# Kernel tuning notes

Hardware: AMD Instinct MI355X
Metric: run time of the kernel (lower is better)

## Reference

```python
import jax, jax.numpy as jnp
import numpy as np

CUTOFF = 5.0
ENV_EXP = 5          # envelope_exponent
NUM_RADIAL = 6
EMB = 128
NUM_ATOM_TYPES = 95
N_NODES = 50000
N_EDGES = 800000


def envelope(x):
    # p = exponent + 1
    p = ENV_EXP + 1
    a = -(p + 1) * (p + 2) / 2.0
    b = p * (p + 2) * 1.0
    c = -p * (p + 1) / 2.0
    x_p_0 = x ** (p - 1)
    x_p_1 = x_p_0 * x
    x_p_2 = x_p_1 * x
    return 1.0 / x + a * x_p_0 + b * x_p_1 + c * x_p_2


def setup_inputs() -> dict:
    key = jax.random.key(0)
    ks = jax.random.split(key, 10)
    Z = jax.random.randint(ks[0], (N_NODES,), 0, NUM_ATOM_TYPES)
    src = jax.random.randint(ks[1], (N_EDGES,), 0, N_NODES)
    dst = jax.random.randint(ks[2], (N_EDGES,), 0, N_NODES)
    rbf = jax.random.normal(ks[3], (N_EDGES, NUM_RADIAL), dtype=jnp.float32)
    # distances in (0, cutoff]; keep away from 0 to avoid 1/x blowup
    d = jax.random.uniform(ks[4], (N_EDGES,), dtype=jnp.float32,
                           minval=0.05, maxval=1.0) * CUTOFF
    sqrt3 = float(np.sqrt(3.0))
    emb_table = jax.random.uniform(ks[5], (NUM_ATOM_TYPES, EMB),
                                   dtype=jnp.float32, minval=-sqrt3, maxval=sqrt3)
    W_rbf = jax.random.normal(ks[6], (EMB, NUM_RADIAL), dtype=jnp.float32) * (1.0 / np.sqrt(NUM_RADIAL))
    b_rbf = jnp.zeros((EMB,), dtype=jnp.float32)
    W_dense = jax.random.normal(ks[7], (EMB, 3 * EMB), dtype=jnp.float32) * (1.0 / np.sqrt(3 * EMB))
    b_dense = jnp.zeros((EMB,), dtype=jnp.float32)
    return {"Z": Z, "src": src, "dst": dst, "rbf": rbf, "d": d,
            "emb_table": emb_table, "W_rbf": W_rbf, "b_rbf": b_rbf,
            "W_dense": W_dense, "b_dense": b_dense}


def reference(Z, src, dst, rbf, d, emb_table, W_rbf, b_rbf, W_dense, b_dense):
    act = jax.nn.silu
    # node embeddings: g.ndata['h'] = embedding(Z)
    h = emb_table[Z]                                   # [N, EMB]
    # edge_init
    rbf_proj = act(rbf @ W_rbf.T + b_rbf)              # [E, EMB]
    m = jnp.concatenate([h[src], h[dst], rbf_proj], axis=-1)  # [E, 3*EMB]
    m = act(m @ W_dense.T + b_dense)                   # [E, EMB]
    d_scaled = d / CUTOFF                              # [E]
    # bessel funcs: sin(n*pi*x)/x, n = 1..NUM_RADIAL (stacked along dim=1)
    freqs = jnp.pi * jnp.arange(1, NUM_RADIAL + 1, dtype=d.dtype)  # [R]
    rbf_env = jnp.sin(d_scaled[:, None] * freqs) / d_scaled[:, None]  # [E, R]
    d_cutoff = envelope(d_scaled)                      # [E]
    rbf_env = d_cutoff[:, None] * rbf_env              # [E, R]
    return h, m, rbf_env
```

## Files before the change

kernel.cpp:

```cpp
#include <hip/hip_runtime.h>
#include <hip/hip_bf16.h>
#include <math.h>

#define CUTOFFV 5.0f
#define NRAD 6
#define EMB 128
#define NTYPES 95
#define PI_F 3.14159265358979323846f

typedef short short8 __attribute__((ext_vector_type(8)));
typedef float f32x4 __attribute__((ext_vector_type(4)));
typedef float f32x2 __attribute__((ext_vector_type(2)));

__device__ __forceinline__ unsigned short f2bf(float f) {
    union { float f; unsigned int u; } v; v.f = f;
    unsigned int u = v.u;
    unsigned int r = (u + 0x7FFFu + ((u >> 16) & 1u)) >> 16;
    return (unsigned short)r;
}

__device__ __forceinline__ short bf16s(float f) {
    union { __hip_bfloat16 h; short s; } u;
    u.h = __float2bfloat16(f);
    return u.s;
}

__device__ __forceinline__ float fast_rcp(float x) {
    float y;
    asm("v_rcp_f32 %0, %1" : "=v"(y) : "v"(x));
    return y;
}

__device__ __forceinline__ float silu_f(float x) {
    return x * fast_rcp(1.0f + __expf(-x));
}

__device__ __forceinline__ void lds_barrier() {
    __builtin_amdgcn_sched_barrier(0);
    asm volatile("s_waitcnt lgkmcnt(0)\n\ts_barrier" ::: "memory");
    __builtin_amdgcn_sched_barrier(0);
}

__global__ void prep_kernel(const float* __restrict__ emb,
                            const float* __restrict__ Wd,
                            const float* __restrict__ bd,
                            const float* __restrict__ Wr,
                            const float* __restrict__ brbf,
                            float* __restrict__ P1, float* __restrict__ P2,
                            unsigned short* __restrict__ W3b,
                            float* __restrict__ Wrp) {
    int b = blockIdx.x, tid = threadIdx.x;
    if (b < 2 * NTYPES) {
        int t = b / NTYPES, z = b % NTYPES;
        __shared__ float emb_s[EMB];
        emb_s[tid] = emb[z * EMB + tid];
        __syncthreads();
        float acc = (t == 0) ? bd[tid] : 0.0f;
        const float* wrow = Wd + (size_t)tid * 384 + t * EMB;
        #pragma unroll 8
        for (int j = 0; j < EMB; ++j) acc += emb_s[j] * wrow[j];
        (t == 0 ? P1 : P2)[z * EMB + tid] = acc;
    } else if (b < 2 * NTYPES + 8) {
        int g = (b - 2 * NTYPES) * 128 + tid;
        for (int i = g; i < EMB * EMB; i += 8 * 128) {
            int n = i >> 7, k = i & 127;
            W3b[i] = f2bf(Wd[(size_t)n * 384 + 256 + k]);
        }
    } else {
        if (tid < EMB) {
            int k = tid;
            #pragma unroll
            for (int j = 0; j < 6; ++j) Wrp[k * 8 + j] = Wr[k * 6 + j];
            Wrp[k * 8 + 6] = brbf[k];
            Wrp[k * 8 + 7] = 0.0f;
        }
    }
}

__global__ void __launch_bounds__(256, 4)
edge_kernel(const int* __restrict__ Z, const int* __restrict__ src,
            const int* __restrict__ dst, const float* __restrict__ rbf,
            const float* __restrict__ dvec, const float* __restrict__ emb,
            const float* __restrict__ P1, const float* __restrict__ P2,
            const unsigned short* __restrict__ W3b,
            const float* __restrict__ Wrp,
            float* __restrict__ out_h, float* __restrict__ out_m,
            float* __restrict__ out_env,
            int N, int E, int ntiles) {
    __shared__ unsigned char A_lds[2][64 * 256];
    __shared__ int zs_s[2][64], zd_s[2][64];

    const int tid = threadIdx.x;
    const int lane = tid & 63;
    const int w = tid >> 6;
    const int lr = lane & 15;
    const int lg = lane >> 4;
    const int wu = __builtin_amdgcn_readfirstlane(w);

    {
        const int total_h = N * (EMB / 4);
        const f32x4* e4 = (const f32x4*)emb;
        for (int idx = blockIdx.x * 256 + tid; idx < total_h;
             idx += gridDim.x * 256) {
            int v = idx >> 5, c = idx & 31;
            __builtin_nontemporal_store(e4[Z[v] * 32 + c], (f32x4*)out_h + idx);
        }
    }
    for (int e = blockIdx.x * 256 + tid; e < E; e += gridDim.x * 256) {
        float x = dvec[e] * (1.0f / CUTOFFV);
        float inv = fast_rcp(x);
        float x2 = x * x;
        float x5 = x2 * x2 * x;
        float env = inv + x5 * (-28.0f + x * (48.0f - 21.0f * x));
        float s1, c1;
        __sincosf(PI_F * x, &s1, &c1);
        float twoc = 2.0f * c1;
        float f = env * inv;
        float s2 = twoc * s1;
        float s3 = twoc * s2 - s1;
        float s4 = twoc * s3 - s2;
        float s5 = twoc * s4 - s3;
        float s6 = twoc * s5 - s4;
        float* o = out_env + (size_t)e * 6;
        __builtin_nontemporal_store((f32x2){f * s1, f * s2}, (f32x2*)o);
        __builtin_nontemporal_store((f32x2){f * s3, f * s4}, (f32x2*)(o + 2));
        __builtin_nontemporal_store((f32x2){f * s5, f * s6}, (f32x2*)(o + 4));
    }

    short8 wfrag[2][4];
    #pragma unroll
    for (int nt = 0; nt < 2; ++nt) {
        int n = w * 32 + nt * 16 + lr;
        #pragma unroll
        for (int ks = 0; ks < 4; ++ks)
            wfrag[nt][ks] = *(const short8*)(W3b + n * EMB + ks * 32 + lg * 8);
    }

    for (int i = 0; ; ++i) {
        const int tp = blockIdx.x + i * gridDim.x;
        const int tc = tp - gridDim.x;
        const bool do_p = (tp < ntiles);
        const bool do_c = (i > 0) && (tc < ntiles);
        if (!do_p && !do_c) break;
        const int pi = i & 1, ci = pi ^ 1;

        f32x2 ra = {0.f, 0.f}, rb = {0.f, 0.f}, rc = {0.f, 0.f};
        int iv = 0;
        if (do_p) {
            const int e0p = tp * 64;
            int ecl = e0p + lane; if (ecl >= E) ecl = E - 1;
            const f32x2* r2 = (const f32x2*)(rbf + (size_t)ecl * 6);
            ra = r2[0]; rb = r2[1]; rc = r2[2];
            if (tid < 128) {
                int ec = e0p + (tid & 63); if (ec >= E) ec = E - 1;
                iv = (tid < 64) ? src[ec] : dst[ec];
            }
        }

        f32x4 o[4][2];
        if (do_c) {
            const unsigned char* Ab = A_lds[ci];
            #pragma unroll
            for (int et = 0; et < 4; ++et) {
                const int e_row = et * 16 + lr;
                short8 bfrag[4];
                #pragma unroll
                for (int ks = 0; ks < 4; ++ks) {
                    int off = (e_row * 256 + (ks * 32 + lg * 8) * 2) ^ ((e_row & 7) << 4);
                    bfrag[ks] = *(const short8*)(Ab + off);
                }
                f32x4 acc[2];
                acc[0] = (f32x4){0.f, 0.f, 0.f, 0.f};
                acc[1] = (f32x4){0.f, 0.f, 0.f, 0.f};
                #pragma unroll
                for (int ks = 0; ks < 4; ++ks)
                    #pragma unroll
                    for (int nt = 0; nt < 2; ++nt)
                        acc[nt] = __builtin_amdgcn_mfma_f32_16x16x32_bf16(
                            wfrag[nt][ks], bfrag[ks], acc[nt], 0, 0, 0);

                const int el = e_row;
                const int zs = zs_s[ci][el], zd = zd_s[ci][el];
                #pragma unroll
                for (int nt = 0; nt < 2; ++nt) {
                    int n4 = w * 32 + nt * 16 + lg * 4;
                    const f32x4 p1 = *(const f32x4*)(P1 + zs * EMB + n4);
                    const f32x4 p2 = *(const f32x4*)(P2 + zd * EMB + n4);
                    f32x4 v;
                    v.x = silu_f(acc[nt][0] + p1.x + p2.x);
                    v.y = silu_f(acc[nt][1] + p1.y + p2.y);
                    v.z = silu_f(acc[nt][2] + p1.z + p2.z);
                    v.w = silu_f(acc[nt][3] + p1.w + p2.w);
                    o[et][nt] = v;
                }
            }
        }

        if (do_p) {
            int zreg = 0;
            if (tid < 128) zreg = Z[iv];

            #pragma unroll
            for (int c = 0; c < 4; ++c) {
                const float* wp0 = Wrp + (size_t)(wu * 32 + c * 8) * 8;
                short8 pk;
                #pragma unroll
                for (int j = 0; j < 8; ++j) {
                    const float* wp = wp0 + j * 8;
                    float pre = wp[6] + ra.x * wp[0] + ra.y * wp[1] +
                                rb.x * wp[2] + rb.y * wp[3] +
                                rc.x * wp[4] + rc.y * wp[5];
                    pk[j] = bf16s(silu_f(pre));
                }
                int k0 = wu * 32 + c * 8;
                int off = (lane * 256 + k0 * 2) ^ ((lane & 7) << 4);
                *(short8*)(A_lds[pi] + off) = pk;
            }

            if (tid < 64) zs_s[pi][tid] = zreg;
            else if (tid < 128) zd_s[pi][tid - 64] = zreg;
        }

        lds_barrier();

        if (do_c) {
            const int e0c = tc * 64;
            unsigned char* Sb = (unsigned char*)A_lds[ci];
            #pragma unroll
            for (int p = 0; p < 2; ++p) {
                #pragma unroll
                for (int q = 0; q < 2; ++q) {
                    const int epass = q * 16 + lr;
                    const int swz = (lr & 7) << 4;
                    #pragma unroll
                    for (int nt = 0; nt < 2; ++nt) {
                        int addr = epass * 512 + ((w * 128 + nt * 64 + lg * 16) ^ swz);
                        *(f32x4*)(Sb + addr) = o[2 * p + q][nt];
                    }
                }
                lds_barrier();
                #pragma unroll
                for (int s = 0; s < 4; ++s) {
                    const int epass = s * 8 + (tid >> 5);
                    const int within = (tid & 31) * 16;
                    const int rd = epass * 512 + (within ^ ((epass & 7) << 4));
                    f32x4 v = *(const f32x4*)(Sb + rd);
                    const int ge = e0c + p * 32 + epass;
                    if (ge < E)
                        __builtin_nontemporal_store(
                            v, (f32x4*)(out_m + (size_t)ge * EMB + (tid & 31) * 4));
                }
                lds_barrier();
            }
        }
    }
}

extern "C" void kernel_launch(void* const* d_in, const int* in_sizes, int n_in,
                              void* d_out, int out_size, void* d_ws, size_t ws_size,
                              hipStream_t stream) {
    const int* Z = (const int*)d_in[0];
    const int* src = (const int*)d_in[1];
    const int* dst = (const int*)d_in[2];
    const float* rbf = (const float*)d_in[3];
    const float* dvec = (const float*)d_in[4];
    const float* emb = (const float*)d_in[5];
    const float* Wr = (const float*)d_in[6];
    const float* brbf = (const float*)d_in[7];
    const float* Wd = (const float*)d_in[8];
    const float* bd = (const float*)d_in[9];

    const int N = in_sizes[0];
    const int E = in_sizes[1];

    float* out_h = (float*)d_out;
    float* out_m = out_h + (size_t)N * EMB;
    float* out_env = out_m + (size_t)E * EMB;

    float* P1 = (float*)d_ws;
    float* P2 = P1 + NTYPES * EMB;
    unsigned short* W3b = (unsigned short*)(P2 + NTYPES * EMB);
    float* Wrp = (float*)(W3b + EMB * EMB);

    prep_kernel<<<2 * NTYPES + 9, 128, 0, stream>>>(emb, Wd, bd, Wr, brbf,
                                                    P1, P2, W3b, Wrp);

    int ntiles = (E + 63) / 64;
    int grid = ntiles < 1024 ? ntiles : 1024;
    edge_kernel<<<grid, 256, 0, stream>>>(Z, src, dst, rbf, dvec, emb,
                                          P1, P2, W3b, Wrp,
                                          out_h, out_m, out_env,
                                          N, E, ntiles);
}
```

Baseline: 155.1 us.

## Use 512-thread blocks and split each 64-edge tile across two wave groups

Doubles the block size to 8 waves. The 64-edge tile is now split so each wave group of four handles 32 edges while keeping its 32-column weight slice. The rbf projection is spread across all 8 waves at 16 columns each, and the out_m staging writes half-tiles per wave group. The aim is more concurrent waves per tile to hide gather and store latency. In exchange, the stricter launch bounds may squeeze registers, and larger blocks synchronise more threads at each barrier.

```diff
diff --git a/kernel.cpp b/kernel.cpp
--- a/kernel.cpp
+++ b/kernel.cpp
@@ -77,7 +77,7 @@
     }
 }
 
-__global__ void __launch_bounds__(256, 4)
+__global__ void __launch_bounds__(512, 8)
 edge_kernel(const int* __restrict__ Z, const int* __restrict__ src,
             const int* __restrict__ dst, const float* __restrict__ rbf,
             const float* __restrict__ dvec, const float* __restrict__ emb,
@@ -95,18 +95,20 @@
     const int w = tid >> 6;
     const int lr = lane & 15;
     const int lg = lane >> 4;
+    const int wn = w & 3;
+    const int we = w >> 2;
     const int wu = __builtin_amdgcn_readfirstlane(w);
 
     {
         const int total_h = N * (EMB / 4);
         const f32x4* e4 = (const f32x4*)emb;
-        for (int idx = blockIdx.x * 256 + tid; idx < total_h;
-             idx += gridDim.x * 256) {
+        for (int idx = blockIdx.x * 512 + tid; idx < total_h;
+             idx += gridDim.x * 512) {
             int v = idx >> 5, c = idx & 31;
             __builtin_nontemporal_store(e4[Z[v] * 32 + c], (f32x4*)out_h + idx);
         }
     }
-    for (int e = blockIdx.x * 256 + tid; e < E; e += gridDim.x * 256) {
+    for (int e = blockIdx.x * 512 + tid; e < E; e += gridDim.x * 512) {
         float x = dvec[e] * (1.0f / CUTOFFV);
         float inv = fast_rcp(x);
         float x2 = x * x;
@@ -130,7 +132,7 @@
     short8 wfrag[2][4];
     #pragma unroll
     for (int nt = 0; nt < 2; ++nt) {
-        int n = w * 32 + nt * 16 + lr;
+        int n = wn * 32 + nt * 16 + lr;
         #pragma unroll
         for (int ks = 0; ks < 4; ++ks)
             wfrag[nt][ks] = *(const short8*)(W3b + n * EMB + ks * 32 + lg * 8);
@@ -157,12 +159,12 @@
             }
         }
 
-        f32x4 o[4][2];
+        f32x4 o[2][2];
         if (do_c) {
             const unsigned char* Ab = A_lds[ci];
             #pragma unroll
-            for (int et = 0; et < 4; ++et) {
-                const int e_row = et * 16 + lr;
+            for (int et = 0; et < 2; ++et) {
+                const int e_row = we * 32 + et * 16 + lr;
                 short8 bfrag[4];
                 #pragma unroll
                 for (int ks = 0; ks < 4; ++ks) {
@@ -183,7 +185,7 @@
                 const int zs = zs_s[ci][el], zd = zd_s[ci][el];
                 #pragma unroll
                 for (int nt = 0; nt < 2; ++nt) {
-                    int n4 = w * 32 + nt * 16 + lg * 4;
+                    int n4 = wn * 32 + nt * 16 + lg * 4;
                     const f32x4 p1 = *(const f32x4*)(P1 + zs * EMB + n4);
                     const f32x4 p2 = *(const f32x4*)(P2 + zd * EMB + n4);
                     f32x4 v;
@@ -201,8 +203,8 @@
             if (tid < 128) zreg = Z[iv];
 
             #pragma unroll
-            for (int c = 0; c < 4; ++c) {
-                const float* wp0 = Wrp + (size_t)(wu * 32 + c * 8) * 8;
+            for (int c = 0; c < 2; ++c) {
+                const float* wp0 = Wrp + (size_t)(wu * 16 + c * 8) * 8;
                 short8 pk;
                 #pragma unroll
                 for (int j = 0; j < 8; ++j) {
@@ -212,7 +214,7 @@
                                 rc.x * wp[4] + rc.y * wp[5];
                     pk[j] = bf16s(silu_f(pre));
                 }
-                int k0 = wu * 32 + c * 8;
+                int k0 = wu * 16 + c * 8;
                 int off = (lane * 256 + k0 * 2) ^ ((lane & 7) << 4);
                 *(short8*)(A_lds[pi] + off) = pk;
             }
@@ -228,27 +230,34 @@
             unsigned char* Sb = (unsigned char*)A_lds[ci];
             #pragma unroll
             for (int p = 0; p < 2; ++p) {
-                #pragma unroll
-                for (int q = 0; q < 2; ++q) {
-                    const int epass = q * 16 + lr;
-                    const int swz = (lr & 7) << 4;
+                if (we == p) {
                     #pragma unroll
-                    for (int nt = 0; nt < 2; ++nt) {
-                        int addr = epass * 512 + ((w * 128 + nt * 64 + lg * 16) ^ swz);
-                        *(f32x4*)(Sb + addr) = o[2 * p + q][nt];
+                    for (int et = 0; et < 2; ++et) {
+                        const int epass = et * 16 + lr;
+                        const int swz = (lr & 7) << 4;
+                        #pragma unroll
+                        for (int nt = 0; nt < 2; ++nt) {
+                            int addr = epass * 512 +
+                                       ((wn * 128 + nt * 64 + lg * 16) ^ swz);
+                            *(f32x4*)(Sb + addr) = o[et][nt];
+                        }
                     }
                 }
                 lds_barrier();
-                #pragma unroll
-                for (int s = 0; s < 4; ++s) {
-                    const int epass = s * 8 + (tid >> 5);
-                    const int within = (tid & 31) * 16;
-                    const int rd = epass * 512 + (within ^ ((epass & 7) << 4));
-                    f32x4 v = *(const f32x4*)(Sb + rd);
+                {
+                    const int epass = tid >> 4;
+                    const int base = (tid & 15) * 32;
                     const int ge = e0c + p * 32 + epass;
-                    if (ge < E)
-                        __builtin_nontemporal_store(
-                            v, (f32x4*)(out_m + (size_t)ge * EMB + (tid & 31) * 4));
+                    #pragma unroll
+                    for (int c16 = 0; c16 < 2; ++c16) {
+                        int rd = epass * 512 +
+                                 ((base + c16 * 16) ^ ((epass & 7) << 4));
+                        f32x4 v = *(const f32x4*)(Sb + rd);
+                        if (ge < E)
+                            __builtin_nontemporal_store(
+                                v, (f32x4*)(out_m + (size_t)ge * EMB +
+                                            (base >> 2) + c16 * 4));
+                    }
                 }
                 lds_barrier();
             }
@@ -287,7 +296,7 @@
 
     int ntiles = (E + 63) / 64;
     int grid = ntiles < 1024 ? ntiles : 1024;
-    edge_kernel<<<grid, 256, 0, stream>>>(Z, src, dst, rbf, dvec, emb,
+    edge_kernel<<<grid, 512, 0, stream>>>(Z, src, dst, rbf, dvec, emb,
                                           P1, P2, W3b, Wrp,
                                           out_h, out_m, out_env,
                                           N, E, ntiles);
```

After: 394.2 us. 2.54x slower.
